# Kernel optimization log

Measured on AMD Instinct MI355X. Metric: run time of the kernel, lower is better.

The kernel has to match this reference:

```python
import jax, jax.numpy as jnp
import numpy as np
from jax import lax

DIM = 64
HID = int(DIM * 2.67)  # 170, matches torch int(dim*ffn_expansion_factor)
EPS_LN = 1e-5
EPS_NORM = 1e-12


def _conv1x1(x, w, b):
    # x: [B,C,H,W], w: [O,C], b: [O]
    return jnp.einsum('oc,bchw->bohw', w, x) + b[None, :, None, None]


def _dwconv3(x, w, b):
    # depthwise 3x3, w: [C,1,3,3]
    y = lax.conv_general_dilated(x, w, (1, 1), 'SAME',
                                 dimension_numbers=('NCHW', 'OIHW', 'NCHW'),
                                 feature_group_count=x.shape[1])
    return y + b[None, :, None, None]


def _ln_channel(x, w, b):
    # WithBias LayerNorm over channel dim (torch does to_3d then LN over c)
    mu = jnp.mean(x, axis=1, keepdims=True)
    var = jnp.mean((x - mu) ** 2, axis=1, keepdims=True)
    return (x - mu) / jnp.sqrt(var + EPS_LN) * w[None, :, None, None] + b[None, :, None, None]


def _l2norm(x):
    n = jnp.sqrt(jnp.sum(x * x, axis=-1, keepdims=True))
    return x / jnp.maximum(n, EPS_NORM)


def _attn_wxw(x, ln_w, ln_b, qkv_w, qkv_b, dw_w, dw_b, pw, pb, temp):
    m = x
    y = _ln_channel(x, ln_w, ln_b)
    qkv = _dwconv3(_conv1x1(y, qkv_w, qkv_b), dw_w, dw_b)
    q, k, v = jnp.split(qkv, 3, axis=1)
    B, C, H, W = q.shape
    q2 = _l2norm(q.reshape(B, C * H, W))  # 'b c h w -> b (c h) w', normalize over w
    k2 = _l2norm(k.reshape(B, C * H, W))
    attn = jax.nn.softmax(jnp.einsum('bnw,bnu->bwu', q2, k2) * temp[0, 0], axis=-1)  # [B,W,W]
    out = jnp.einsum('bchw,bwu->bchu', v, attn)  # v @ attn with broadcast head dim
    return _conv1x1(out, pw, pb) + m


def _attn_hxh(x, ln_w, ln_b, qkv_w, qkv_b, dw_w, dw_b, pw, pb, temp):
    m = x
    y = _ln_channel(x, ln_w, ln_b)
    qkv = _dwconv3(_conv1x1(y, qkv_w, qkv_b), dw_w, dw_b)
    q, k, v = jnp.split(qkv, 3, axis=1)
    B, C, H, W = q.shape
    q2 = _l2norm(jnp.transpose(q, (0, 2, 1, 3)).reshape(B, H, C * W))  # 'b c h w -> b h (c w)'
    k2 = _l2norm(jnp.transpose(k, (0, 2, 1, 3)).reshape(B, H, C * W))
    attn = jax.nn.softmax(jnp.einsum('bhn,bgn->bhg', q2, k2) * temp[0, 0], axis=-1)  # [B,H,H]
    out = jnp.einsum('bhg,bcgw->bchw', attn, v)  # attn @ v with broadcast head dim
    return _conv1x1(out, pw, pb) + m


def _ffn(x, in_w, in_b, dw_w, dw_b, out_w, out_b):
    y = _dwconv3(_conv1x1(x, in_w, in_b), dw_w, dw_b)
    x1, x2 = jnp.split(y, 2, axis=1)
    return _conv1x1(jax.nn.gelu(x1, approximate=False) * x2, out_w, out_b)


def setup_inputs() -> dict:
    key = jax.random.key(0)
    ks = iter(jax.random.split(key, 32))
    B, C, H, W = 4, DIM, 256, 256
    s = 0.02

    def nrm(shape):
        return jax.random.normal(next(ks), shape, dtype=jnp.float32) * s

    d = {
        'x': jax.random.normal(next(ks), (B, C, H, W), dtype=jnp.float32),
        'zero_map': jnp.ones((B, 1, H, W), dtype=jnp.float32),
    }
    for p in ('w', 'h'):
        d[p + '_ln_w'] = jnp.ones((C,), jnp.float32)
        d[p + '_ln_b'] = jnp.zeros((C,), jnp.float32)
        d[p + '_qkv_w'] = nrm((3 * C, C))
        d[p + '_qkv_b'] = jnp.zeros((3 * C,), jnp.float32)
        d[p + '_dw_w'] = nrm((3 * C, 1, 3, 3))
        d[p + '_dw_b'] = jnp.zeros((3 * C,), jnp.float32)
        d[p + '_proj_w'] = nrm((C, C))
        d[p + '_proj_b'] = jnp.zeros((C,), jnp.float32)
        d[p + '_temp'] = jnp.ones((1, 1), jnp.float32)
    d['n2_w'] = jnp.ones((C,), jnp.float32)
    d['n2_b'] = jnp.zeros((C,), jnp.float32)
    d['ffn_in_w'] = nrm((2 * HID, C))
    d['ffn_in_b'] = jnp.zeros((2 * HID,), jnp.float32)
    d['ffn_dw_w'] = nrm((2 * HID, 1, 3, 3))
    d['ffn_dw_b'] = jnp.zeros((2 * HID,), jnp.float32)
    d['ffn_out_w'] = nrm((C, HID))
    d['ffn_out_b'] = jnp.zeros((C,), jnp.float32)
    return d


def reference(x, zero_map,
              w_ln_w, w_ln_b, w_qkv_w, w_qkv_b, w_dw_w, w_dw_b, w_proj_w, w_proj_b, w_temp,
              h_ln_w, h_ln_b, h_qkv_w, h_qkv_b, h_dw_w, h_dw_b, h_proj_w, h_proj_b, h_temp,
              n2_w, n2_b,
              ffn_in_w, ffn_in_b, ffn_dw_w, ffn_dw_b, ffn_out_w, ffn_out_b):
    # DeepTransformerBlock_withnoZeromap.forward (zero_map is unused in the torch code)
    m = _attn_wxw(x, w_ln_w, w_ln_b, w_qkv_w, w_qkv_b, w_dw_w, w_dw_b, w_proj_w, w_proj_b, w_temp)
    z = _attn_hxh(m, h_ln_w, h_ln_b, h_qkv_w, h_qkv_b, h_dw_w, h_dw_b, h_proj_w, h_proj_b, h_temp)
    return z + _ffn(_ln_channel(z, n2_w, n2_b), ffn_in_w, ffn_in_b, ffn_dw_w, ffn_dw_b, ffn_out_w, ffn_out_b)
```

## Files before the change

### kernel.cpp

```cpp
#include <hip/hip_runtime.h>
#include <math.h>
#include <stdint.h>

#define P_ 65536

#define DW_OFF   0ul
#define QKV_OFF  12582912ul
#define ATTP_OFF QKV_OFF
#define Y_OFF    25165824ul
#define ATT_OFF  31457280ul
#define HID_OFF  0ul
#define G_OFF    22282240ul
#define WSB      33423360ul

typedef __attribute__((ext_vector_type(8))) short bf16x8;
typedef __attribute__((ext_vector_type(4))) float f32x4;

__device__ __forceinline__ unsigned short f2bf(float f) {
    uint32_t u = __float_as_uint(f);
    return (unsigned short)((u + 0x7FFFu + ((u >> 16) & 1u)) >> 16);
}
__device__ __forceinline__ float bf2f(unsigned short h) {
    return __uint_as_float((uint32_t)h << 16);
}

template<int CIN, int CPAD, int COUT, int COPAD, int PX, bool LN, bool RES>
__global__ __launch_bounds__(256) void conv_mfma_kernel(
        const float* __restrict__ in_, const float* __restrict__ lnw,
        const float* __restrict__ lnb, const float* __restrict__ Wt,
        const float* __restrict__ bias, float* __restrict__ out_,
        const float* __restrict__ res_, size_t zi, size_t zo, size_t zr) {
    constexpr int NSL = CPAD / 32;
    constexpr int NMT = PX / 16;
    constexpr bool HOIST = (CPAD == 64 && PX == 128);
    const float* in = in_ + (size_t)blockIdx.z * zi;
    float* out = out_ + (size_t)blockIdx.z * zo;
    const float* res = nullptr;
    if constexpr (RES) res = res_ + (size_t)blockIdx.z * zr;
    __shared__ unsigned short sX[PX * CPAD];
    __shared__ unsigned short sW[COPAD * CPAD];
    __shared__ float sPa[256], sPb[256], sMu[128], sInv[128];
    int tid = threadIdx.x;
    int hw0 = blockIdx.x * PX;
    int obase = blockIdx.y * COPAD;
    int lane = tid & 63, wave = tid >> 6;

    {
        uint32_t* sX32 = (uint32_t*)sX;
        #pragma unroll
        for (int it = 0; it < PX * CPAD / 512; ++it) {
            int idx = tid + it * 256;
            int p = idx & (PX - 1), c = (idx / PX) * 2;
            float v0 = (c < CIN)     ? in[(size_t)c * P_ + hw0 + p]     : 0.f;
            float v1 = (c + 1 < CIN) ? in[(size_t)(c+1) * P_ + hw0 + p] : 0.f;
            uint32_t pk = (uint32_t)f2bf(v0) | ((uint32_t)f2bf(v1) << 16);
            int kb = c >> 3;
            sX32[(p * CPAD + (((kb ^ (p & 7)) << 3) | (c & 7))) >> 1] = pk;
        }
    }
    {
        uint32_t* sW32 = (uint32_t*)sW;
        #pragma unroll
        for (int it = 0; it < COPAD * CPAD / 512; ++it) {
            int idx = tid + it * 256;
            int c2 = idx % (CPAD / 2), o = idx / (CPAD / 2);
            int c = c2 * 2, og = obase + o;
            float v0 = (og < COUT && c < CIN)     ? Wt[(size_t)og * CIN + c]     : 0.f;
            float v1 = (og < COUT && c + 1 < CIN) ? Wt[(size_t)og * CIN + c + 1] : 0.f;
            uint32_t pk = (uint32_t)f2bf(v0) | ((uint32_t)f2bf(v1) << 16);
            int kb = c >> 3;
            sW32[(o * CPAD + (((kb ^ (o & 7)) << 3) | (c & 7))) >> 1] = pk;
        }
    }
    __syncthreads();
    if constexpr (LN) {
        static_assert(!LN || (CPAD == 64 && PX == 128), "LN path assumes 64ch/128px");
        int p = tid & 127, q = tid >> 7;
        float s = 0.f, s2 = 0.f;
        #pragma unroll
        for (int c = q * 32; c < q * 32 + 32; ++c) {
            float v = bf2f(sX[p * 64 + ((((c >> 3) ^ (p & 7)) << 3) | (c & 7))]);
            s += v; s2 += v * v;
        }
        sPa[tid] = s; sPb[tid] = s2;
        __syncthreads();
        if (tid < 128) {
            float ss = sPa[tid] + sPa[tid+128];
            float qq = sPb[tid] + sPb[tid+128];
            float mu = ss * (1.f/64.f);
            float var = qq * (1.f/64.f) - mu * mu;
            sMu[tid] = mu; sInv[tid] = rsqrtf(var + 1e-5f);
        }
        __syncthreads();
        float mu = sMu[p], inv = sInv[p];
        #pragma unroll
        for (int c = q * 32; c < q * 32 + 32; ++c) {
            int sw = p * 64 + ((((c >> 3) ^ (p & 7)) << 3) | (c & 7));
            float v = bf2f(sX[sw]);
            sX[sw] = f2bf((v - mu) * inv * lnw[c] + lnb[c]);
        }
        __syncthreads();
    }

    int pxl = lane & 15, quad = lane >> 4;
    int olim = (COUT - obase < COPAD) ? (COUT - obase) : COPAD;
    int ntile = (olim + 15) >> 4;
    bf16x8 xf[HOIST ? NMT * NSL : 1];
    if constexpr (HOIST) {
        #pragma unroll
        for (int m = 0; m < NMT; ++m)
            #pragma unroll
            for (int s = 0; s < NSL; ++s) {
                int p = m * 16 + pxl;
                int kb = s * 4 + quad;
                xf[m * NSL + s] = *(const bf16x8*)&sX[p * CPAD + ((kb ^ (p & 7)) << 3)];
            }
    }
    for (int ot = wave; ot < ntile; ot += 4) {
        int on = ot * 16 + pxl;
        int og = obase + on;
        f32x4 acc[NMT];
        #pragma unroll
        for (int m = 0; m < NMT; ++m) acc[m] = (f32x4){0.f, 0.f, 0.f, 0.f};
        #pragma unroll
        for (int s = 0; s < NSL; ++s) {
            int kb = s * 4 + quad;
            bf16x8 wf = *(const bf16x8*)&sW[on * CPAD + ((kb ^ (on & 7)) << 3)];
            #pragma unroll
            for (int m = 0; m < NMT; ++m) {
                bf16x8 af;
                if constexpr (HOIST) af = xf[m * NSL + s];
                else {
                    int p = m * 16 + pxl;
                    af = *(const bf16x8*)&sX[p * CPAD + ((kb ^ (p & 7)) << 3)];
                }
                acc[m] = __builtin_amdgcn_mfma_f32_16x16x32_bf16(af, wf, acc[m], 0, 0, 0);
            }
        }
        bool oval = og < COUT;
        float bv = oval ? bias[og] : 0.f;
        #pragma unroll
        for (int m = 0; m < NMT; ++m) {
            if (oval) {
                size_t ob = (size_t)og * P_ + hw0 + m * 16 + quad * 4;
                float4 v = make_float4(acc[m][0] + bv, acc[m][1] + bv,
                                       acc[m][2] + bv, acc[m][3] + bv);
                if constexpr (RES) {
                    float4 rv = *(const float4*)&res[ob];
                    v.x += rv.x; v.y += rv.y; v.z += rv.z; v.w += rv.w;
                }
                *(float4*)&out[ob] = v;
            }
        }
    }
}

__device__ __forceinline__ void mfma_step64(const unsigned short* sA,
        const unsigned short* sB, int wave, int lane, f32x4 acc[2][8]) {
    int pxl = lane & 15, quad = lane >> 4;
    #pragma unroll
    for (int s = 0; s < 2; ++s) {
        int kb = s * 4 + quad;
        bf16x8 af[2];
        #pragma unroll
        for (int mt = 0; mt < 2; ++mt) {
            int im = wave * 32 + mt * 16 + pxl;
            af[mt] = *(const bf16x8*)&sA[im * 64 + ((kb ^ (im & 7)) << 3)];
        }
        #pragma unroll
        for (int jt = 0; jt < 8; ++jt) {
            int jn = jt * 16 + pxl;
            bf16x8 bf = *(const bf16x8*)&sB[jn * 64 + ((kb ^ (jn & 7)) << 3)];
            #pragma unroll
            for (int mt = 0; mt < 2; ++mt)
                acc[mt][jt] = __builtin_amdgcn_mfma_f32_16x16x32_bf16(af[mt], bf, acc[mt][jt], 0, 0, 0);
        }
    }
}

#define STAGE_DIRECT64(sDst, ROWADDR, Q)                                     \
    {   uint32_t* s32_ = (uint32_t*)(sDst);                                  \
        _Pragma("unroll")                                                    \
        for (int it_ = 0; it_ < 8; ++it_) {                                  \
            int idx_ = tid + it_ * 256;                                      \
            int il_ = idx_ >> 4, k_ = (idx_ & 15) * 4;                       \
            float4 v_ = *(const float4*)(ROWADDR(il_) + (Q) * 64 + k_);      \
            uint32_t p0_ = (uint32_t)f2bf(v_.x) | ((uint32_t)f2bf(v_.y) << 16); \
            uint32_t p1_ = (uint32_t)f2bf(v_.z) | ((uint32_t)f2bf(v_.w) << 16); \
            int off_ = il_ * 64 + ((((k_ >> 3) ^ (il_ & 7)) << 3) | (k_ & 7)); \
            s32_[off_ >> 1] = p0_;                                           \
            s32_[(off_ >> 1) + 1] = p1_;                                     \
        }                                                                    \
    }

#define STAGE_TRANS64(sDst, KROWADDR, Q)                                     \
    {   _Pragma("unroll")                                                    \
        for (int it_ = 0; it_ < 8; ++it_) {                                  \
            int idx_ = tid + it_ * 256;                                      \
            int r_ = idx_ >> 5, il4_ = (idx_ & 31) * 4;                      \
            float4 v_ = *(const float4*)(KROWADDR((Q) * 64 + r_) + il4_);    \
            float vv_[4] = {v_.x, v_.y, v_.z, v_.w};                         \
            int kb_ = r_ >> 3;                                               \
            _Pragma("unroll")                                                \
            for (int e_ = 0; e_ < 4; ++e_) {                                 \
                int il_ = il4_ + e_;                                         \
                (sDst)[il_ * 64 + (((kb_ ^ (il_ & 7)) << 3) | (r_ & 7))] = f2bf(vv_[e_]); \
            }                                                                \
        }                                                                    \
    }

template<bool HXH>
__global__ __launch_bounds__(256) void attn_logits_mfma(const float* __restrict__ dw_,
        float* __restrict__ part_, size_t zd, size_t zp) {
    __shared__ unsigned short sA[128 * 64];
    __shared__ unsigned short sB[128 * 64];
    const float* dw = dw_ + (size_t)blockIdx.z * zd;
    float* part = part_ + (size_t)blockIdx.z * zp;
    int tid = threadIdx.x, lane = tid & 63, wave = tid >> 6;
    int i0 = (blockIdx.x & 1) * 128, j0 = (blockIdx.x >> 1) * 128;
    int ks = blockIdx.y;
    const float* qc = dw + ((size_t)ks << 16);
    const float* kc = dw + ((size_t)(64 + ks) << 16);
    f32x4 acc[2][8];
    #pragma unroll
    for (int mt = 0; mt < 2; ++mt)
        #pragma unroll
        for (int jt = 0; jt < 8; ++jt) acc[mt][jt] = (f32x4){0.f, 0.f, 0.f, 0.f};
    for (int q = 0; q < 4; ++q) {
        if (q) __syncthreads();
        if constexpr (HXH) {
            #define ROWA_Q(il) (qc + (size_t)(i0 + (il)) * 256)
            #define ROWA_K(il) (kc + (size_t)(j0 + (il)) * 256)
            STAGE_DIRECT64(sA, ROWA_Q, q)
            STAGE_DIRECT64(sB, ROWA_K, q)
            #undef ROWA_Q
            #undef ROWA_K
        } else {
            #define KROW_Q(r) (qc + (size_t)(r) * 256 + i0)
            #define KROW_K(r) (kc + (size_t)(r) * 256 + j0)
            STAGE_TRANS64(sA, KROW_Q, q)
            STAGE_TRANS64(sB, KROW_K, q)
            #undef KROW_Q
            #undef KROW_K
        }
        __syncthreads();
        mfma_step64(sA, sB, wave, lane, acc);
    }
    int pxl = lane & 15, quad = lane >> 4;
    float* pb = part + ((size_t)ks << 16);
    #pragma unroll
    for (int mt = 0; mt < 2; ++mt) {
        #pragma unroll
        for (int jt = 0; jt < 8; ++jt) {
            #pragma unroll
            for (int r = 0; r < 4; ++r) {
                int i = i0 + wave * 32 + mt * 16 + quad * 4 + r;
                int j = j0 + jt * 16 + pxl;
                pb[(size_t)i * 256 + j] = acc[mt][jt][r];
            }
        }
    }
}

__global__ __launch_bounds__(256) void av_w_mfma(const float* __restrict__ dw_,
        const float* __restrict__ att_, float* __restrict__ out_,
        size_t zd, size_t za, size_t zo) {
    __shared__ unsigned short sA[128 * 64];
    __shared__ unsigned short sB[128 * 64];
    const float* dw = dw_ + (size_t)blockIdx.z * zd;
    const float* att = att_ + (size_t)blockIdx.z * za;
    float* out = out_ + (size_t)blockIdx.z * zo;
    int tid = threadIdx.x, lane = tid & 63, wave = tid >> 6;
    int m0 = blockIdx.x * 128, u0 = blockIdx.y * 128;
    f32x4 acc[2][8];
    #pragma unroll
    for (int mt = 0; mt < 2; ++mt)
        #pragma unroll
        for (int jt = 0; jt < 8; ++jt) acc[mt][jt] = (f32x4){0.f, 0.f, 0.f, 0.f};
    for (int q = 0; q < 4; ++q) {
        if (q) __syncthreads();
        #define ROWA_V(il) (dw + ((size_t)(128 + ((m0 + (il)) & 63)) << 16) \
                               + ((m0 + (il)) >> 6) * 256)
        #define KROW_ATT(r) (att + (size_t)(r) * 256 + u0)
        STAGE_DIRECT64(sA, ROWA_V, q)
        STAGE_TRANS64(sB, KROW_ATT, q)
        #undef ROWA_V
        #undef KROW_ATT
        __syncthreads();
        mfma_step64(sA, sB, wave, lane, acc);
    }
    int pxl = lane & 15, quad = lane >> 4;
    #pragma unroll
    for (int mt = 0; mt < 2; ++mt) {
        #pragma unroll
        for (int jt = 0; jt < 8; ++jt) {
            #pragma unroll
            for (int r = 0; r < 4; ++r) {
                int m = m0 + wave * 32 + mt * 16 + quad * 4 + r;
                int c = m & 63, h = m >> 6;
                out[((size_t)c << 16) + h * 256 + u0 + jt * 16 + pxl] = acc[mt][jt][r];
            }
        }
    }
}

__global__ __launch_bounds__(256) void av_h_mfma(const float* __restrict__ dw_,
        const float* __restrict__ att_, float* __restrict__ out_,
        size_t zd, size_t za, size_t zo) {
    __shared__ unsigned short sA[128 * 64];
    __shared__ unsigned short sB[128 * 64];
    const float* dw = dw_ + (size_t)blockIdx.z * zd;
    const float* att = att_ + (size_t)blockIdx.z * za;
    float* out = out_ + (size_t)blockIdx.z * zo;
    int tid = threadIdx.x, lane = tid & 63, wave = tid >> 6;
    int c = blockIdx.x >> 1;
    int w0 = (blockIdx.x & 1) * 128;
    int h0 = blockIdx.y * 128;
    const float* vc = dw + ((size_t)(128 + c) << 16);
    f32x4 acc[2][8];
    #pragma unroll
    for (int mt = 0; mt < 2; ++mt)
        #pragma unroll
        for (int jt = 0; jt < 8; ++jt) acc[mt][jt] = (f32x4){0.f, 0.f, 0.f, 0.f};
    for (int q = 0; q < 4; ++q) {
        if (q) __syncthreads();
        #define ROWA_ATT(il) (att + (size_t)(h0 + (il)) * 256)
        #define KROW_V(r) (vc + (size_t)(r) * 256 + w0)
        STAGE_DIRECT64(sA, ROWA_ATT, q)
        STAGE_TRANS64(sB, KROW_V, q)
        #undef ROWA_ATT
        #undef KROW_V
        __syncthreads();
        mfma_step64(sA, sB, wave, lane, acc);
    }
    int pxl = lane & 15, quad = lane >> 4;
    #pragma unroll
    for (int mt = 0; mt < 2; ++mt) {
        #pragma unroll
        for (int jt = 0; jt < 8; ++jt) {
            #pragma unroll
            for (int r = 0; r < 4; ++r) {
                int h = h0 + wave * 32 + mt * 16 + quad * 4 + r;
                out[((size_t)c << 16) + h * 256 + w0 + jt * 16 + pxl] = acc[mt][jt][r];
            }
        }
    }
}

__global__ __launch_bounds__(256) void softmax_kernel(const float* __restrict__ part_,
        const float* __restrict__ temp, float* __restrict__ att_,
        size_t zp, size_t za) {
    const float* part = part_ + (size_t)blockIdx.z * zp;
    float* att = att_ + (size_t)blockIdx.z * za;
    int i = blockIdx.x;
    int j = threadIdx.x;
    size_t rowoff = (size_t)i * 256 + j;
    float s = 0.f;
    #pragma unroll
    for (int kk = 0; kk < 64; ++kk) s += part[(size_t)kk * 65536 + rowoff];
    s *= temp[0];
    __shared__ float redA[4], redB[4];
    int wv = j >> 6, ln = j & 63;
    float m = s;
    #pragma unroll
    for (int off = 32; off; off >>= 1) m = fmaxf(m, __shfl_down(m, off, 64));
    if (ln == 0) redA[wv] = m;
    __syncthreads();
    m = fmaxf(fmaxf(redA[0], redA[1]), fmaxf(redA[2], redA[3]));
    float e = expf(s - m);
    float t2 = e;
    #pragma unroll
    for (int off = 32; off; off >>= 1) t2 += __shfl_down(t2, off, 64);
    if (ln == 0) redB[wv] = t2;
    __syncthreads();
    float tot = redB[0] + redB[1] + redB[2] + redB[3];
    att[rowoff] = e / tot;
}

template<bool NORM>
__global__ __launch_bounds__(256) void dw_row_kernel(const float* __restrict__ in_,
        const float* __restrict__ w9, const float* __restrict__ bias,
        float* __restrict__ out_, size_t zi, size_t zo) {
    const float* in = in_ + (size_t)blockIdx.z * zi;
    float* out = out_ + (size_t)blockIdx.z * zo;
    int row = __builtin_amdgcn_readfirstlane(blockIdx.x * 4 + (threadIdx.x >> 6));
    int o = row >> 8, h = row & 255;
    int lane = threadIdx.x & 63;
    const float* ip = in + ((size_t)o << 16);
    const float* wp = w9 + o * 9;
    float b = bias[o];
    float4 acc = make_float4(b, b, b, b);
    #pragma unroll
    for (int dy = -1; dy <= 1; ++dy) {
        int hh = h + dy;
        float4 v = make_float4(0.f, 0.f, 0.f, 0.f);
        if (hh >= 0 && hh <= 255)
            v = *(const float4*)(ip + hh * 256 + lane * 4);
        float lft = __shfl(v.w, lane - 1);
        float rgt = __shfl(v.x, lane + 1);
        if (lane == 0)  lft = 0.f;
        if (lane == 63) rgt = 0.f;
        float w0 = wp[(dy+1)*3], w1 = wp[(dy+1)*3+1], w2 = wp[(dy+1)*3+2];
        acc.x += w0*lft + w1*v.x + w2*v.y;
        acc.y += w0*v.x + w1*v.y + w2*v.z;
        acc.z += w0*v.y + w1*v.z + w2*v.w;
        acc.w += w0*v.z + w1*v.w + w2*rgt;
    }
    if constexpr (NORM) {
        if (o < 128) {
            float s = acc.x*acc.x + acc.y*acc.y + acc.z*acc.z + acc.w*acc.w;
            #pragma unroll
            for (int off = 32; off; off >>= 1) s += __shfl_xor(s, off, 64);
            float inv = 1.0f / fmaxf(sqrtf(s), 1e-12f);
            acc.x *= inv; acc.y *= inv; acc.z *= inv; acc.w *= inv;
        }
    }
    *(float4*)(out + ((size_t)o << 16) + h * 256 + lane * 4) = acc;
}

__global__ __launch_bounds__(256) void ffn_dw_row_kernel(const float* __restrict__ hid_,
        const float* __restrict__ w9, const float* __restrict__ bias,
        float* __restrict__ g_, size_t zi, size_t zo) {
    const float* hid = hid_ + (size_t)blockIdx.z * zi;
    float* g = g_ + (size_t)blockIdx.z * zo;
    int row = __builtin_amdgcn_readfirstlane(blockIdx.x * 4 + (threadIdx.x >> 6));
    int i = row >> 8, h = row & 255;
    int lane = threadIdx.x & 63;
    const float* ip1 = hid + ((size_t)i << 16);
    const float* ip2 = ip1 + ((size_t)170 << 16);
    const float* wp1 = w9 + i * 9;
    const float* wp2 = w9 + (i + 170) * 9;
    float ba = bias[i], bb = bias[i + 170];
    float4 a = make_float4(ba, ba, ba, ba);
    float4 c = make_float4(bb, bb, bb, bb);
    #pragma unroll
    for (int dy = -1; dy <= 1; ++dy) {
        int hh = h + dy;
        float4 v1 = make_float4(0.f, 0.f, 0.f, 0.f);
        float4 v2 = make_float4(0.f, 0.f, 0.f, 0.f);
        if (hh >= 0 && hh <= 255) {
            v1 = *(const float4*)(ip1 + hh * 256 + lane * 4);
            v2 = *(const float4*)(ip2 + hh * 256 + lane * 4);
        }
        float l1 = __shfl(v1.w, lane - 1), r1 = __shfl(v1.x, lane + 1);
        float l2 = __shfl(v2.w, lane - 1), r2 = __shfl(v2.x, lane + 1);
        if (lane == 0)  { l1 = 0.f; l2 = 0.f; }
        if (lane == 63) { r1 = 0.f; r2 = 0.f; }
        float u0 = wp1[(dy+1)*3], u1 = wp1[(dy+1)*3+1], u2 = wp1[(dy+1)*3+2];
        float q0 = wp2[(dy+1)*3], q1 = wp2[(dy+1)*3+1], q2 = wp2[(dy+1)*3+2];
        a.x += u0*l1   + u1*v1.x + u2*v1.y;
        a.y += u0*v1.x + u1*v1.y + u2*v1.z;
        a.z += u0*v1.y + u1*v1.z + u2*v1.w;
        a.w += u0*v1.z + u1*v1.w + u2*r1;
        c.x += q0*l2   + q1*v2.x + q2*v2.y;
        c.y += q0*v2.x + q1*v2.y + q2*v2.z;
        c.z += q0*v2.y + q1*v2.z + q2*v2.w;
        c.w += q0*v2.z + q1*v2.w + q2*r2;
    }
    const float ISQ2 = 0.70710678118654752440f;
    float4 r;
    r.x = 0.5f * a.x * (1.0f + erff(a.x * ISQ2)) * c.x;
    r.y = 0.5f * a.y * (1.0f + erff(a.y * ISQ2)) * c.y;
    r.z = 0.5f * a.z * (1.0f + erff(a.z * ISQ2)) * c.z;
    r.w = 0.5f * a.w * (1.0f + erff(a.w * ISQ2)) * c.w;
    *(float4*)(g + ((size_t)i << 16) + h * 256 + lane * 4) = r;
}

__global__ __launch_bounds__(256) void l2norm_h_kernel(float* __restrict__ dw_,
        size_t zd) {
    float* dw = dw_ + (size_t)blockIdx.z * zd;
    int h = blockIdx.x, qk = blockIdx.y;
    float* base = dw + ((size_t)(qk*64) << 16) + h*256;
    int tid = threadIdx.x;
    float s = 0.f;
    for (int idx = tid; idx < 16384; idx += 256) {
        int c = idx >> 8, w = idx & 255;
        float v = base[((size_t)c << 16) + w];
        s += v * v;
    }
    #pragma unroll
    for (int off = 32; off; off >>= 1) s += __shfl_down(s, off, 64);
    __shared__ float red[4];
    int wv = tid >> 6, ln = tid & 63;
    if (ln == 0) red[wv] = s;
    __syncthreads();
    float tot = red[0] + red[1] + red[2] + red[3];
    float inv = 1.0f / fmaxf(sqrtf(tot), 1e-12f);
    for (int idx = tid; idx < 16384; idx += 256) {
        int c = idx >> 8, w = idx & 255;
        base[((size_t)c << 16) + w] *= inv;
    }
}

extern "C" void kernel_launch(void* const* d_in, const int* in_sizes, int n_in,
                              void* d_out, int out_size, void* d_ws, size_t ws_size,
                              hipStream_t stream) {
    (void)in_sizes; (void)n_in; (void)out_size;
    const float* x = (const float*)d_in[0];
    float* ws  = (float*)d_ws;
    float* out = (float*)d_out;
    const size_t XB = (size_t)64 * P_;
    const size_t SLAB_BYTES = WSB * sizeof(float);
    int nb = 1;
    if (ws_size >= 4 * SLAB_BYTES) nb = 4;
    else if (ws_size >= 2 * SLAB_BYTES) nb = 2;

    for (int b0 = 0; b0 < 4; b0 += nb) {
        int zc = (4 - b0 < nb) ? (4 - b0) : nb;
        const float* xb = x + (size_t)b0 * XB;
        float* outb = out + (size_t)b0 * XB;
        float* DW   = ws + DW_OFF;
        float* QKV  = ws + QKV_OFF;
        float* ATTP = ws + ATTP_OFF;
        float* Y    = ws + Y_OFF;
        float* ATT  = ws + ATT_OFF;
        float* HID  = ws + HID_OFF;
        float* G    = ws + G_OFF;

        conv_mfma_kernel<64,64,192,192,128,true,false><<<dim3(512,1,zc), 256, 0, stream>>>(
                xb, (const float*)d_in[2], (const float*)d_in[3],
                (const float*)d_in[4], (const float*)d_in[5], QKV, nullptr,
                XB, WSB, 0);
        dw_row_kernel<true><<<dim3(12288,1,zc), 256, 0, stream>>>(QKV,
                (const float*)d_in[6], (const float*)d_in[7], DW, WSB, WSB);
        attn_logits_mfma<false><<<dim3(4,64,zc), 256, 0, stream>>>(DW, ATTP, WSB, WSB);
        softmax_kernel<<<dim3(256,1,zc), 256, 0, stream>>>(ATTP,
                (const float*)d_in[10], ATT, WSB, WSB);
        av_w_mfma<<<dim3(128,2,zc), 256, 0, stream>>>(DW, ATT, Y, WSB, WSB, WSB);
        conv_mfma_kernel<64,64,64,64,128,false,true><<<dim3(512,1,zc), 256, 0, stream>>>(
                Y, nullptr, nullptr,
                (const float*)d_in[8], (const float*)d_in[9], outb, xb,
                WSB, XB, XB);

        conv_mfma_kernel<64,64,192,192,128,true,false><<<dim3(512,1,zc), 256, 0, stream>>>(
                outb, (const float*)d_in[11], (const float*)d_in[12],
                (const float*)d_in[13], (const float*)d_in[14], QKV, nullptr,
                XB, WSB, 0);
        dw_row_kernel<false><<<dim3(12288,1,zc), 256, 0, stream>>>(QKV,
                (const float*)d_in[15], (const float*)d_in[16], DW, WSB, WSB);
        l2norm_h_kernel<<<dim3(256,2,zc), 256, 0, stream>>>(DW, WSB);
        attn_logits_mfma<true><<<dim3(4,64,zc), 256, 0, stream>>>(DW, ATTP, WSB, WSB);
        softmax_kernel<<<dim3(256,1,zc), 256, 0, stream>>>(ATTP,
                (const float*)d_in[19], ATT, WSB, WSB);
        av_h_mfma<<<dim3(128,2,zc), 256, 0, stream>>>(DW, ATT, Y, WSB, WSB, WSB);
        conv_mfma_kernel<64,64,64,64,128,false,true><<<dim3(512,1,zc), 256, 0, stream>>>(
                Y, nullptr, nullptr,
                (const float*)d_in[17], (const float*)d_in[18], outb, outb,
                WSB, XB, XB);

        conv_mfma_kernel<64,64,340,192,128,true,false><<<dim3(512,2,zc), 256, 0, stream>>>(
                outb, (const float*)d_in[20], (const float*)d_in[21],
                (const float*)d_in[22], (const float*)d_in[23], HID, nullptr,
                XB, WSB, 0);
        ffn_dw_row_kernel<<<dim3(10880,1,zc), 256, 0, stream>>>(HID,
                (const float*)d_in[24], (const float*)d_in[25], G, WSB, WSB);
        conv_mfma_kernel<170,192,64,64,64,false,true><<<dim3(1024,1,zc), 256, 0, stream>>>(
                G, nullptr, nullptr,
                (const float*)d_in[26], (const float*)d_in[27], outb, outb,
                WSB, XB, XB);
    }
}
```

Baseline: 1.345 ms.

## Store intermediate activations in bf16 to halve memory traffic between kernels

The QKV, depthwise-conv, attention-output, FFN hidden and gated intermediates are now stored as bf16 in the workspace instead of fp32. Producer kernels round on write and consumer kernels read ushort4 and widen, or stage bf16 straight into shared memory without converting. This halves global read/write bytes in a memory-bound pipeline. It also re-tiles the QKV and FFN-in convs to 128 output channels per block with more blocks in y. The cost is extra rounding error in the intermediates (l2norm now rewrites values in place at bf16), and the attention logits and softmax stay fp32.

```diff
diff --git a/kernel.cpp b/kernel.cpp
--- a/kernel.cpp
+++ b/kernel.cpp
@@ -13,33 +13,33 @@
 #define G_OFF    22282240ul
 #define WSB      33423360ul
 
+typedef unsigned short ush;
 typedef __attribute__((ext_vector_type(8))) short bf16x8;
 typedef __attribute__((ext_vector_type(4))) float f32x4;
 
-__device__ __forceinline__ unsigned short f2bf(float f) {
+__device__ __forceinline__ ush f2bf(float f) {
     uint32_t u = __float_as_uint(f);
-    return (unsigned short)((u + 0x7FFFu + ((u >> 16) & 1u)) >> 16);
-}
-__device__ __forceinline__ float bf2f(unsigned short h) {
+    return (ush)((u + 0x7FFFu + ((u >> 16) & 1u)) >> 16);
+}
+__device__ __forceinline__ float bf2f(ush h) {
     return __uint_as_float((uint32_t)h << 16);
 }
 
-template<int CIN, int CPAD, int COUT, int COPAD, int PX, bool LN, bool RES>
+template<int CIN, int CPAD, int COUT, int COPAD, int PX, bool LN, bool RES,
+         bool INBF, bool OUTBF>
 __global__ __launch_bounds__(256) void conv_mfma_kernel(
-        const float* __restrict__ in_, const float* __restrict__ lnw,
+        const void* __restrict__ in_, const float* __restrict__ lnw,
         const float* __restrict__ lnb, const float* __restrict__ Wt,
-        const float* __restrict__ bias, float* __restrict__ out_,
+        const float* __restrict__ bias, void* __restrict__ out_,
         const float* __restrict__ res_, size_t zi, size_t zo, size_t zr) {
+    static_assert(!(RES && OUTBF), "res only with fp32 out");
     constexpr int NSL = CPAD / 32;
     constexpr int NMT = PX / 16;
     constexpr bool HOIST = (CPAD == 64 && PX == 128);
-    const float* in = in_ + (size_t)blockIdx.z * zi;
-    float* out = out_ + (size_t)blockIdx.z * zo;
-    const float* res = nullptr;
-    if constexpr (RES) res = res_ + (size_t)blockIdx.z * zr;
-    __shared__ unsigned short sX[PX * CPAD];
-    __shared__ unsigned short sW[COPAD * CPAD];
-    __shared__ float sPa[256], sPb[256], sMu[128], sInv[128];
+    __shared__ ush sX[PX * CPAD];
+    __shared__ ush sW[COPAD * CPAD];
+    __shared__ float sPa[LN ? 256 : 1], sPb[LN ? 256 : 1];
+    __shared__ float sMu[LN ? 128 : 1], sInv[LN ? 128 : 1];
     int tid = threadIdx.x;
     int hw0 = blockIdx.x * PX;
     int obase = blockIdx.y * COPAD;
@@ -51,9 +51,18 @@
         for (int it = 0; it < PX * CPAD / 512; ++it) {
             int idx = tid + it * 256;
             int p = idx & (PX - 1), c = (idx / PX) * 2;
-            float v0 = (c < CIN)     ? in[(size_t)c * P_ + hw0 + p]     : 0.f;
-            float v1 = (c + 1 < CIN) ? in[(size_t)(c+1) * P_ + hw0 + p] : 0.f;
-            uint32_t pk = (uint32_t)f2bf(v0) | ((uint32_t)f2bf(v1) << 16);
+            uint32_t pk;
+            if constexpr (INBF) {
+                const ush* in = (const ush*)in_ + (size_t)blockIdx.z * zi;
+                ush a = (c < CIN)     ? in[(size_t)c * P_ + hw0 + p]     : (ush)0;
+                ush b = (c + 1 < CIN) ? in[(size_t)(c+1) * P_ + hw0 + p] : (ush)0;
+                pk = (uint32_t)a | ((uint32_t)b << 16);
+            } else {
+                const float* in = (const float*)in_ + (size_t)blockIdx.z * zi;
+                float v0 = (c < CIN)     ? in[(size_t)c * P_ + hw0 + p]     : 0.f;
+                float v1 = (c + 1 < CIN) ? in[(size_t)(c+1) * P_ + hw0 + p] : 0.f;
+                pk = (uint32_t)f2bf(v0) | ((uint32_t)f2bf(v1) << 16);
+            }
             int kb = c >> 3;
             sX32[(p * CPAD + (((kb ^ (p & 7)) << 3) | (c & 7))) >> 1] = pk;
         }
@@ -143,20 +152,30 @@
         for (int m = 0; m < NMT; ++m) {
             if (oval) {
                 size_t ob = (size_t)og * P_ + hw0 + m * 16 + quad * 4;
-                float4 v = make_float4(acc[m][0] + bv, acc[m][1] + bv,
-                                       acc[m][2] + bv, acc[m][3] + bv);
-                if constexpr (RES) {
-                    float4 rv = *(const float4*)&res[ob];
-                    v.x += rv.x; v.y += rv.y; v.z += rv.z; v.w += rv.w;
+                if constexpr (OUTBF) {
+                    ush* out = (ush*)out_ + (size_t)blockIdx.z * zo;
+                    ushort4 sv;
+                    sv.x = f2bf(acc[m][0] + bv); sv.y = f2bf(acc[m][1] + bv);
+                    sv.z = f2bf(acc[m][2] + bv); sv.w = f2bf(acc[m][3] + bv);
+                    *(ushort4*)&out[ob] = sv;
+                } else {
+                    float* out = (float*)out_ + (size_t)blockIdx.z * zo;
+                    float4 v = make_float4(acc[m][0] + bv, acc[m][1] + bv,
+                                           acc[m][2] + bv, acc[m][3] + bv);
+                    if constexpr (RES) {
+                        const float* res = res_ + (size_t)blockIdx.z * zr;
+                        float4 rv = *(const float4*)&res[ob];
+                        v.x += rv.x; v.y += rv.y; v.z += rv.z; v.w += rv.w;
+                    }
+                    *(float4*)&out[ob] = v;
                 }
-                *(float4*)&out[ob] = v;
             }
         }
     }
 }
 
-__device__ __forceinline__ void mfma_step64(const unsigned short* sA,
-        const unsigned short* sB, int wave, int lane, f32x4 acc[2][8]) {
+__device__ __forceinline__ void mfma_step64(const ush* sA,
+        const ush* sB, int wave, int lane, f32x4 acc[2][8]) {
     int pxl = lane & 15, quad = lane >> 4;
     #pragma unroll
     for (int s = 0; s < 2; ++s) {
@@ -209,18 +228,45 @@
         }                                                                    \
     }
 
+#define STAGE_DIRECT64_BF(sDst, ROWADDR, Q)                                  \
+    {   _Pragma("unroll")                                                    \
+        for (int it_ = 0; it_ < 8; ++it_) {                                  \
+            int idx_ = tid + it_ * 256;                                      \
+            int il_ = idx_ >> 4, k_ = (idx_ & 15) * 4;                       \
+            ushort4 v_ = *(const ushort4*)(ROWADDR(il_) + (Q) * 64 + k_);    \
+            int off_ = il_ * 64 + ((((k_ >> 3) ^ (il_ & 7)) << 3) | (k_ & 7)); \
+            *(ushort4*)&(sDst)[off_] = v_;                                   \
+        }                                                                    \
+    }
+
+#define STAGE_TRANS64_BF(sDst, KROWADDR, Q)                                  \
+    {   _Pragma("unroll")                                                    \
+        for (int it_ = 0; it_ < 8; ++it_) {                                  \
+            int idx_ = tid + it_ * 256;                                      \
+            int r_ = idx_ >> 5, il4_ = (idx_ & 31) * 4;                      \
+            ushort4 v_ = *(const ushort4*)(KROWADDR((Q) * 64 + r_) + il4_);  \
+            ush vv_[4] = {v_.x, v_.y, v_.z, v_.w};                          \
+            int kb_ = r_ >> 3;                                               \
+            _Pragma("unroll")                                                \
+            for (int e_ = 0; e_ < 4; ++e_) {                                 \
+                int il_ = il4_ + e_;                                         \
+                (sDst)[il_ * 64 + (((kb_ ^ (il_ & 7)) << 3) | (r_ & 7))] = vv_[e_]; \
+            }                                                                \
+        }                                                                    \
+    }
+
 template<bool HXH>
-__global__ __launch_bounds__(256) void attn_logits_mfma(const float* __restrict__ dw_,
+__global__ __launch_bounds__(256) void attn_logits_mfma(const ush* __restrict__ dw_,
         float* __restrict__ part_, size_t zd, size_t zp) {
-    __shared__ unsigned short sA[128 * 64];
-    __shared__ unsigned short sB[128 * 64];
-    const float* dw = dw_ + (size_t)blockIdx.z * zd;
+    __shared__ ush sA[128 * 64];
+    __shared__ ush sB[128 * 64];
+    const ush* dw = dw_ + (size_t)blockIdx.z * zd;
     float* part = part_ + (size_t)blockIdx.z * zp;
     int tid = threadIdx.x, lane = tid & 63, wave = tid >> 6;
     int i0 = (blockIdx.x & 1) * 128, j0 = (blockIdx.x >> 1) * 128;
     int ks = blockIdx.y;
-    const float* qc = dw + ((size_t)ks << 16);
-    const float* kc = dw + ((size_t)(64 + ks) << 16);
+    const ush* qc = dw + ((size_t)ks << 16);
+    const ush* kc = dw + ((size_t)(64 + ks) << 16);
     f32x4 acc[2][8];
     #pragma unroll
     for (int mt = 0; mt < 2; ++mt)
@@ -231,15 +277,15 @@
         if constexpr (HXH) {
             #define ROWA_Q(il) (qc + (size_t)(i0 + (il)) * 256)
             #define ROWA_K(il) (kc + (size_t)(j0 + (il)) * 256)
-            STAGE_DIRECT64(sA, ROWA_Q, q)
-            STAGE_DIRECT64(sB, ROWA_K, q)
+            STAGE_DIRECT64_BF(sA, ROWA_Q, q)
+            STAGE_DIRECT64_BF(sB, ROWA_K, q)
             #undef ROWA_Q
             #undef ROWA_K
         } else {
             #define KROW_Q(r) (qc + (size_t)(r) * 256 + i0)
             #define KROW_K(r) (kc + (size_t)(r) * 256 + j0)
-            STAGE_TRANS64(sA, KROW_Q, q)
-            STAGE_TRANS64(sB, KROW_K, q)
+            STAGE_TRANS64_BF(sA, KROW_Q, q)
+            STAGE_TRANS64_BF(sB, KROW_K, q)
             #undef KROW_Q
             #undef KROW_K
         }
@@ -262,14 +308,14 @@
     }
 }
 
-__global__ __launch_bounds__(256) void av_w_mfma(const float* __restrict__ dw_,
-        const float* __restrict__ att_, float* __restrict__ out_,
+__global__ __launch_bounds__(256) void av_w_mfma(const ush* __restrict__ dw_,
+        const float* __restrict__ att_, ush* __restrict__ out_,
         size_t zd, size_t za, size_t zo) {
-    __shared__ unsigned short sA[128 * 64];
-    __shared__ unsigned short sB[128 * 64];
-    const float* dw = dw_ + (size_t)blockIdx.z * zd;
+    __shared__ ush sA[128 * 64];
+    __shared__ ush sB[128 * 64];
+    const ush* dw = dw_ + (size_t)blockIdx.z * zd;
     const float* att = att_ + (size_t)blockIdx.z * za;
-    float* out = out_ + (size_t)blockIdx.z * zo;
+    ush* out = out_ + (size_t)blockIdx.z * zo;
     int tid = threadIdx.x, lane = tid & 63, wave = tid >> 6;
     int m0 = blockIdx.x * 128, u0 = blockIdx.y * 128;
     f32x4 acc[2][8];
@@ -282,7 +328,7 @@
         #define ROWA_V(il) (dw + ((size_t)(128 + ((m0 + (il)) & 63)) << 16) \
                                + ((m0 + (il)) >> 6) * 256)
         #define KROW_ATT(r) (att + (size_t)(r) * 256 + u0)
-        STAGE_DIRECT64(sA, ROWA_V, q)
+        STAGE_DIRECT64_BF(sA, ROWA_V, q)
         STAGE_TRANS64(sB, KROW_ATT, q)
         #undef ROWA_V
         #undef KROW_ATT
@@ -298,25 +344,25 @@
             for (int r = 0; r < 4; ++r) {
                 int m = m0 + wave * 32 + mt * 16 + quad * 4 + r;
                 int c = m & 63, h = m >> 6;
-                out[((size_t)c << 16) + h * 256 + u0 + jt * 16 + pxl] = acc[mt][jt][r];
+                out[((size_t)c << 16) + h * 256 + u0 + jt * 16 + pxl] = f2bf(acc[mt][jt][r]);
             }
         }
     }
 }
 
-__global__ __launch_bounds__(256) void av_h_mfma(const float* __restrict__ dw_,
-        const float* __restrict__ att_, float* __restrict__ out_,
+__global__ __launch_bounds__(256) void av_h_mfma(const ush* __restrict__ dw_,
+        const float* __restrict__ att_, ush* __restrict__ out_,
         size_t zd, size_t za, size_t zo) {
-    __shared__ unsigned short sA[128 * 64];
-    __shared__ unsigned short sB[128 * 64];
-    const float* dw = dw_ + (size_t)blockIdx.z * zd;
+    __shared__ ush sA[128 * 64];
+    __shared__ ush sB[128 * 64];
+    const ush* dw = dw_ + (size_t)blockIdx.z * zd;
     const float* att = att_ + (size_t)blockIdx.z * za;
-    float* out = out_ + (size_t)blockIdx.z * zo;
+    ush* out = out_ + (size_t)blockIdx.z * zo;
     int tid = threadIdx.x, lane = tid & 63, wave = tid >> 6;
     int c = blockIdx.x >> 1;
     int w0 = (blockIdx.x & 1) * 128;
     int h0 = blockIdx.y * 128;
-    const float* vc = dw + ((size_t)(128 + c) << 16);
+    const ush* vc = dw + ((size_t)(128 + c) << 16);
     f32x4 acc[2][8];
     #pragma unroll
     for (int mt = 0; mt < 2; ++mt)
@@ -327,7 +373,7 @@
         #define ROWA_ATT(il) (att + (size_t)(h0 + (il)) * 256)
         #define KROW_V(r) (vc + (size_t)(r) * 256 + w0)
         STAGE_DIRECT64(sA, ROWA_ATT, q)
-        STAGE_TRANS64(sB, KROW_V, q)
+        STAGE_TRANS64_BF(sB, KROW_V, q)
         #undef ROWA_ATT
         #undef KROW_V
         __syncthreads();
@@ -341,7 +387,7 @@
             #pragma unroll
             for (int r = 0; r < 4; ++r) {
                 int h = h0 + wave * 32 + mt * 16 + quad * 4 + r;
-                out[((size_t)c << 16) + h * 256 + w0 + jt * 16 + pxl] = acc[mt][jt][r];
+                out[((size_t)c << 16) + h * 256 + w0 + jt * 16 + pxl] = f2bf(acc[mt][jt][r]);
             }
         }
     }
@@ -378,15 +424,15 @@
 }
 
 template<bool NORM>
-__global__ __launch_bounds__(256) void dw_row_kernel(const float* __restrict__ in_,
+__global__ __launch_bounds__(256) void dw_row_kernel(const ush* __restrict__ in_,
         const float* __restrict__ w9, const float* __restrict__ bias,
-        float* __restrict__ out_, size_t zi, size_t zo) {
-    const float* in = in_ + (size_t)blockIdx.z * zi;
-    float* out = out_ + (size_t)blockIdx.z * zo;
+        ush* __restrict__ out_, size_t zi, size_t zo) {
+    const ush* in = in_ + (size_t)blockIdx.z * zi;
+    ush* out = out_ + (size_t)blockIdx.z * zo;
     int row = __builtin_amdgcn_readfirstlane(blockIdx.x * 4 + (threadIdx.x >> 6));
     int o = row >> 8, h = row & 255;
     int lane = threadIdx.x & 63;
-    const float* ip = in + ((size_t)o << 16);
+    const ush* ip = in + ((size_t)o << 16);
     const float* wp = w9 + o * 9;
     float b = bias[o];
     float4 acc = make_float4(b, b, b, b);
@@ -394,8 +440,10 @@
     for (int dy = -1; dy <= 1; ++dy) {
         int hh = h + dy;
         float4 v = make_float4(0.f, 0.f, 0.f, 0.f);
-        if (hh >= 0 && hh <= 255)
-            v = *(const float4*)(ip + hh * 256 + lane * 4);
+        if (hh >= 0 && hh <= 255) {
+            ushort4 t = *(const ushort4*)(ip + hh * 256 + lane * 4);
+            v = make_float4(bf2f(t.x), bf2f(t.y), bf2f(t.z), bf2f(t.w));
+        }
         float lft = __shfl(v.w, lane - 1);
         float rgt = __shfl(v.x, lane + 1);
         if (lane == 0)  lft = 0.f;
@@ -415,19 +463,21 @@
             acc.x *= inv; acc.y *= inv; acc.z *= inv; acc.w *= inv;
         }
     }
-    *(float4*)(out + ((size_t)o << 16) + h * 256 + lane * 4) = acc;
-}
-
-__global__ __launch_bounds__(256) void ffn_dw_row_kernel(const float* __restrict__ hid_,
+    ushort4 s4;
+    s4.x = f2bf(acc.x); s4.y = f2bf(acc.y); s4.z = f2bf(acc.z); s4.w = f2bf(acc.w);
+    *(ushort4*)(out + ((size_t)o << 16) + h * 256 + lane * 4) = s4;
+}
+
+__global__ __launch_bounds__(256) void ffn_dw_row_kernel(const ush* __restrict__ hid_,
         const float* __restrict__ w9, const float* __restrict__ bias,
-        float* __restrict__ g_, size_t zi, size_t zo) {
-    const float* hid = hid_ + (size_t)blockIdx.z * zi;
-    float* g = g_ + (size_t)blockIdx.z * zo;
+        ush* __restrict__ g_, size_t zi, size_t zo) {
+    const ush* hid = hid_ + (size_t)blockIdx.z * zi;
+    ush* g = g_ + (size_t)blockIdx.z * zo;
     int row = __builtin_amdgcn_readfirstlane(blockIdx.x * 4 + (threadIdx.x >> 6));
     int i = row >> 8, h = row & 255;
     int lane = threadIdx.x & 63;
-    const float* ip1 = hid + ((size_t)i << 16);
-    const float* ip2 = ip1 + ((size_t)170 << 16);
+    const ush* ip1 = hid + ((size_t)i << 16);
+    const ush* ip2 = ip1 + ((size_t)170 << 16);
     const float* wp1 = w9 + i * 9;
     const float* wp2 = w9 + (i + 170) * 9;
     float ba = bias[i], bb = bias[i + 170];
@@ -439,8 +489,10 @@
         float4 v1 = make_float4(0.f, 0.f, 0.f, 0.f);
         float4 v2 = make_float4(0.f, 0.f, 0.f, 0.f);
         if (hh >= 0 && hh <= 255) {
-            v1 = *(const float4*)(ip1 + hh * 256 + lane * 4);
-            v2 = *(const float4*)(ip2 + hh * 256 + lane * 4);
+            ushort4 t1 = *(const ushort4*)(ip1 + hh * 256 + lane * 4);
+            ushort4 t2 = *(const ushort4*)(ip2 + hh * 256 + lane * 4);
+            v1 = make_float4(bf2f(t1.x), bf2f(t1.y), bf2f(t1.z), bf2f(t1.w));
+            v2 = make_float4(bf2f(t2.x), bf2f(t2.y), bf2f(t2.z), bf2f(t2.w));
         }
         float l1 = __shfl(v1.w, lane - 1), r1 = __shfl(v1.x, lane + 1);
         float l2 = __shfl(v2.w, lane - 1), r2 = __shfl(v2.x, lane + 1);
@@ -458,25 +510,26 @@
         c.w += q0*v2.z + q1*v2.w + q2*r2;
     }
     const float ISQ2 = 0.70710678118654752440f;
-    float4 r;
-    r.x = 0.5f * a.x * (1.0f + erff(a.x * ISQ2)) * c.x;
-    r.y = 0.5f * a.y * (1.0f + erff(a.y * ISQ2)) * c.y;
-    r.z = 0.5f * a.z * (1.0f + erff(a.z * ISQ2)) * c.z;
-    r.w = 0.5f * a.w * (1.0f + erff(a.w * ISQ2)) * c.w;
-    *(float4*)(g + ((size_t)i << 16) + h * 256 + lane * 4) = r;
-}
-
-__global__ __launch_bounds__(256) void l2norm_h_kernel(float* __restrict__ dw_,
+    ushort4 s4;
+    s4.x = f2bf(0.5f * a.x * (1.0f + erff(a.x * ISQ2)) * c.x);
+    s4.y = f2bf(0.5f * a.y * (1.0f + erff(a.y * ISQ2)) * c.y);
+    s4.z = f2bf(0.5f * a.z * (1.0f + erff(a.z * ISQ2)) * c.z);
+    s4.w = f2bf(0.5f * a.w * (1.0f + erff(a.w * ISQ2)) * c.w);
+    *(ushort4*)(g + ((size_t)i << 16) + h * 256 + lane * 4) = s4;
+}
+
+__global__ __launch_bounds__(256) void l2norm_h_kernel(ush* __restrict__ dw_,
         size_t zd) {
-    float* dw = dw_ + (size_t)blockIdx.z * zd;
+    ush* dw = dw_ + (size_t)blockIdx.z * zd;
     int h = blockIdx.x, qk = blockIdx.y;
-    float* base = dw + ((size_t)(qk*64) << 16) + h*256;
+    ush* base = dw + ((size_t)(qk*64) << 16) + h*256;
     int tid = threadIdx.x;
     float s = 0.f;
-    for (int idx = tid; idx < 16384; idx += 256) {
-        int c = idx >> 8, w = idx & 255;
-        float v = base[((size_t)c << 16) + w];
-        s += v * v;
+    for (int idx = tid; idx < 4096; idx += 256) {
+        int c = idx >> 6, w4 = (idx & 63) * 4;
+        ushort4 t = *(const ushort4*)&base[((size_t)c << 16) + w4];
+        float a = bf2f(t.x), b = bf2f(t.y), cc = bf2f(t.z), d = bf2f(t.w);
+        s += a*a + b*b + cc*cc + d*d;
     }
     #pragma unroll
     for (int off = 32; off; off >>= 1) s += __shfl_down(s, off, 64);
@@ -486,9 +539,13 @@
     __syncthreads();
     float tot = red[0] + red[1] + red[2] + red[3];
     float inv = 1.0f / fmaxf(sqrtf(tot), 1e-12f);
-    for (int idx = tid; idx < 16384; idx += 256) {
-        int c = idx >> 8, w = idx & 255;
-        base[((size_t)c << 16) + w] *= inv;
+    for (int idx = tid; idx < 4096; idx += 256) {
+        int c = idx >> 6, w4 = (idx & 63) * 4;
+        ushort4 t = *(const ushort4*)&base[((size_t)c << 16) + w4];
+        ushort4 o;
+        o.x = f2bf(bf2f(t.x) * inv); o.y = f2bf(bf2f(t.y) * inv);
+        o.z = f2bf(bf2f(t.z) * inv); o.w = f2bf(bf2f(t.w) * inv);
+        *(ushort4*)&base[((size_t)c << 16) + w4] = o;
     }
 }
 
@@ -500,6 +557,7 @@
     float* ws  = (float*)d_ws;
     float* out = (float*)d_out;
     const size_t XB = (size_t)64 * P_;
+    const size_t WSB2 = 2 * WSB;
     const size_t SLAB_BYTES = WSB * sizeof(float);
     int nb = 1;
     if (ws_size >= 4 * SLAB_BYTES) nb = 4;
@@ -509,54 +567,60 @@
         int zc = (4 - b0 < nb) ? (4 - b0) : nb;
         const float* xb = x + (size_t)b0 * XB;
         float* outb = out + (size_t)b0 * XB;
-        float* DW   = ws + DW_OFF;
-        float* QKV  = ws + QKV_OFF;
+        ush*   DW   = (ush*)(ws + DW_OFF);
+        ush*   QKV  = (ush*)(ws + QKV_OFF);
         float* ATTP = ws + ATTP_OFF;
-        float* Y    = ws + Y_OFF;
+        ush*   Y    = (ush*)(ws + Y_OFF);
         float* ATT  = ws + ATT_OFF;
-        float* HID  = ws + HID_OFF;
-        float* G    = ws + G_OFF;
-
-        conv_mfma_kernel<64,64,192,192,128,true,false><<<dim3(512,1,zc), 256, 0, stream>>>(
+        ush*   HID  = (ush*)(ws + HID_OFF);
+        ush*   G    = (ush*)(ws + G_OFF);
+
+        conv_mfma_kernel<64,64,192,128,128,true,false,false,true>
+            <<<dim3(512,2,zc), 256, 0, stream>>>(
                 xb, (const float*)d_in[2], (const float*)d_in[3],
                 (const float*)d_in[4], (const float*)d_in[5], QKV, nullptr,
-                XB, WSB, 0);
+                XB, WSB2, 0);
         dw_row_kernel<true><<<dim3(12288,1,zc), 256, 0, stream>>>(QKV,
-                (const float*)d_in[6], (const float*)d_in[7], DW, WSB, WSB);
-        attn_logits_mfma<false><<<dim3(4,64,zc), 256, 0, stream>>>(DW, ATTP, WSB, WSB);
+                (const float*)d_in[6], (const float*)d_in[7], DW, WSB2, WSB2);
+        attn_logits_mfma<false><<<dim3(4,64,zc), 256, 0, stream>>>(DW, ATTP, WSB2, WSB);
         softmax_kernel<<<dim3(256,1,zc), 256, 0, stream>>>(ATTP,
                 (const float*)d_in[10], ATT, WSB, WSB);
-        av_w_mfma<<<dim3(128,2,zc), 256, 0, stream>>>(DW, ATT, Y, WSB, WSB, WSB);
-        conv_mfma_kernel<64,64,64,64,128,false,true><<<dim3(512,1,zc), 256, 0, stream>>>(
+        av_w_mfma<<<dim3(128,2,zc), 256, 0, stream>>>(DW, ATT, Y, WSB2, WSB, WSB2);
+        conv_mfma_kernel<64,64,64,64,128,false,true,true,false>
+            <<<dim3(512,1,zc), 256, 0, stream>>>(
                 Y, nullptr, nullptr,
                 (const float*)d_in[8], (const float*)d_in[9], outb, xb,
-                WSB, XB, XB);
-
-        conv_mfma_kernel<64,64,192,192,128,true,false><<<dim3(512,1,zc), 256, 0, stream>>>(
+                WSB2, XB, XB);
+
+        conv_mfma_kernel<64,64,192,128,128,true,false,false,true>
+            <<<dim3(512,2,zc), 256, 0, stream>>>(
                 outb, (const float*)d_in[11], (const float*)d_in[12],
                 (const float*)d_in[13], (const float*)d_in[14], QKV, nullptr,
-                XB, WSB, 0);
+                XB, WSB2, 0);
         dw_row_kernel<false><<<dim3(12288,1,zc), 256, 0, stream>>>(QKV,
-                (const float*)d_in[15], (const float*)d_in[16], DW, WSB, WSB);
-        l2norm_h_kernel<<<dim3(256,2,zc), 256, 0, stream>>>(DW, WSB);
-        attn_logits_mfma<true><<<dim3(4,64,zc), 256, 0, stream>>>(DW, ATTP, WSB, WSB);
+                (const float*)d_in[15], (const float*)d_in[16], DW, WSB2, WSB2);
+        l2norm_h_kernel<<<dim3(256,2,zc), 256, 0, stream>>>(DW, WSB2);
+        attn_logits_mfma<true><<<dim3(4,64,zc), 256, 0, stream>>>(DW, ATTP, WSB2, WSB);
         softmax_kernel<<<dim3(256,1,zc), 256, 0, stream>>>(ATTP,
                 (const float*)d_in[19], ATT, WSB, WSB);
-        av_h_mfma<<<dim3(128,2,zc), 256, 0, stream>>>(DW, ATT, Y, WSB, WSB, WSB);
-        conv_mfma_kernel<64,64,64,64,128,false,true><<<dim3(512,1,zc), 256, 0, stream>>>(
+        av_h_mfma<<<dim3(128,2,zc), 256, 0, stream>>>(DW, ATT, Y, WSB2, WSB, WSB2);
+        conv_mfma_kernel<64,64,64,64,128,false,true,true,false>
+            <<<dim3(512,1,zc), 256, 0, stream>>>(
                 Y, nullptr, nullptr,
                 (const float*)d_in[17], (const float*)d_in[18], outb, outb,
-                WSB, XB, XB);
-
-        conv_mfma_kernel<64,64,340,192,128,true,false><<<dim3(512,2,zc), 256, 0, stream>>>(
+                WSB2, XB, XB);
+
+        conv_mfma_kernel<64,64,340,128,128,true,false,false,true>
+            <<<dim3(512,3,zc), 256, 0, stream>>>(
                 outb, (const float*)d_in[20], (const float*)d_in[21],
                 (const float*)d_in[22], (const float*)d_in[23], HID, nullptr,
-                XB, WSB, 0);
+                XB, WSB2, 0);
         ffn_dw_row_kernel<<<dim3(10880,1,zc), 256, 0, stream>>>(HID,
-                (const float*)d_in[24], (const float*)d_in[25], G, WSB, WSB);
-        conv_mfma_kernel<170,192,64,64,64,false,true><<<dim3(1024,1,zc), 256, 0, stream>>>(
+                (const float*)d_in[24], (const float*)d_in[25], G, WSB2, WSB2);
+        conv_mfma_kernel<170,192,64,64,64,false,true,true,false>
+            <<<dim3(1024,1,zc), 256, 0, stream>>>(
                 G, nullptr, nullptr,
                 (const float*)d_in[26], (const float*)d_in[27], outb, outb,
-                WSB, XB, XB);
-    }
-}
+                WSB2, XB, XB);
+    }
+}
```

Measured after the change: 1.158 ms. 1.16x faster.
